# Performance work log

Hardware: AMD Instinct MI355X
Metric: run time of the kernel (lower is better)

The kernel has to match this reference:

```python
import jax, jax.numpy as jnp
import numpy as np

N_A, N_C, N_L = 50000, 10000, 10000
HID = 128


def _gatv2(x_src, x_dst, src, dst, ea, Wl, bl, Wr, br, We, att, bias, H):
    # GATv2Conv (PyG) bipartite, edge_dim=1, concat=False (mean over heads), eval mode (no dropout)
    C = bias.shape[0]
    n_dst = x_dst.shape[0]
    xl = (x_src @ Wl + bl).reshape(-1, H, C)      # [N_src, H, C]
    xr = (x_dst @ Wr + br).reshape(-1, H, C)      # [N_dst, H, C]
    e = jax.nn.leaky_relu(xl[src] + xr[dst] + (ea @ We).reshape(-1, H, C), 0.2)  # [E,H,C]
    logit = jnp.einsum('ehc,hc->eh', e, att)      # [E,H]
    m = jax.ops.segment_max(logit, dst, num_segments=n_dst)
    m = jax.lax.stop_gradient(jnp.where(jnp.isfinite(m), m, 0.0))
    ex = jnp.exp(logit - m[dst])
    denom = jax.ops.segment_sum(ex, dst, num_segments=n_dst)
    alpha = ex / (denom[dst] + 1e-16)             # segment softmax over incoming edges
    out = jax.ops.segment_sum(alpha[:, :, None] * xl[src], dst, num_segments=n_dst)
    return out.mean(axis=1) + bias                # concat=False -> head mean + bias


def setup_inputs() -> dict:
    key = jax.random.key(0)
    ks = iter(jax.random.split(key, 80))
    def rn(shape, s=1.0):
        return jax.random.normal(next(ks), shape, jnp.float32) * s
    inp = {}
    inp['x_asset'] = rn((N_A, 512))
    inp['x_creator'] = rn((N_C, 2))
    inp['x_licensee'] = rn((N_L, 1))
    # edges: (name, E, src_max, dst_max)
    edges = [('cb', 50000, N_A, N_C), ('lt', 100000, N_A, N_L), ('sim', 200000, N_A, N_A),
             ('fw', 100000, N_A, N_A), ('rcb', 50000, N_C, N_A), ('rlt', 100000, N_L, N_A)]
    for name, E, smax, dmax in edges:
        inp[f'{name}_src'] = jax.random.randint(next(ks), (E,), 0, smax, jnp.int32)
        inp[f'{name}_dst'] = jax.random.randint(next(ks), (E,), 0, dmax, jnp.int32)
        inp[f'ea_{name}'] = rn((E, 1))
    w = 0.05  # param scale
    inp['Wp_a'] = rn((512, HID), w); inp['bp_a'] = rn((HID,), w)
    inp['Wp_c'] = rn((2, HID), w);   inp['bp_c'] = rn((HID,), w)
    inp['Wp_l'] = rn((1, HID), w);   inp['bp_l'] = rn((HID,), w)
    # layer 1: heads=2, stacked over the 6 relations
    H1 = 2
    inp['Wl1'] = rn((6, HID, H1 * HID), w); inp['bl1'] = rn((6, H1 * HID), w)
    inp['Wr1'] = rn((6, HID, H1 * HID), w); inp['br1'] = rn((6, H1 * HID), w)
    inp['We1'] = rn((6, 1, H1 * HID), w)
    inp['att1'] = rn((6, H1, HID), w); inp['bias1'] = rn((6, HID), w)
    # layer 2: heads=1
    inp['Wl2'] = rn((6, HID, HID), w); inp['bl2'] = rn((6, HID), w)
    inp['Wr2'] = rn((6, HID, HID), w); inp['br2'] = rn((6, HID), w)
    inp['We2'] = rn((6, 1, HID), w)
    inp['att2'] = rn((6, 1, HID), w); inp['bias2'] = rn((6, HID), w)
    inp['Wc1'] = rn((HID, HID), w); inp['bc1'] = rn((HID,), w)
    inp['Wc2'] = rn((HID, 3), w);   inp['bc2'] = rn((3,), w)
    inp['query_asset_index'] = 123
    return inp


def reference(x_asset, x_creator, x_licensee, Wp_a, bp_a, Wp_c, bp_c, Wp_l, bp_l,
              Wl1, bl1, Wr1, br1, We1, att1, bias1,
              Wl2, bl2, Wr2, br2, We2, att2, bias2,
              Wc1, bc1, Wc2, bc2,
              ea_cb, ea_lt, ea_sim, ea_fw, ea_rcb, ea_rlt,
              cb_src, cb_dst, lt_src, lt_dst, sim_src, sim_dst,
              fw_src, fw_dst, rcb_src, rcb_dst, rlt_src, rlt_dst,
              query_asset_index):
    x = {'Asset': x_asset @ Wp_a + bp_a,
         'Creator': x_creator @ Wp_c + bp_c,
         'Licensee': x_licensee @ Wp_l + bp_l}
    rels = [('Asset', 'Creator', cb_src, cb_dst, ea_cb),
            ('Asset', 'Licensee', lt_src, lt_dst, ea_lt),
            ('Asset', 'Asset', sim_src, sim_dst, ea_sim),
            ('Asset', 'Asset', fw_src, fw_dst, ea_fw),
            ('Creator', 'Asset', rcb_src, rcb_dst, ea_rcb),
            ('Licensee', 'Asset', rlt_src, rlt_dst, ea_rlt)]

    def hetero_layer(x, Wl, bl, Wr, br, We, att, bias, H):
        out = {k: jnp.zeros((v.shape[0], HID), v.dtype) for k, v in x.items()}
        for i, (st, dt, s, d, ea) in enumerate(rels):  # HeteroConv aggr='sum'
            out[dt] = out[dt] + _gatv2(x[st], x[dt], s, d, ea,
                                       Wl[i], bl[i], Wr[i], br[i], We[i], att[i], bias[i], H)
        return out

    x = hetero_layer(x, Wl1, bl1, Wr1, br1, We1, att1, bias1, 2)
    x = {k: jax.nn.relu(v) for k, v in x.items()}  # eval: dropout is identity
    x = hetero_layer(x, Wl2, bl2, Wr2, br2, We2, att2, bias2, 1)
    x = {k: jax.nn.relu(v) for k, v in x.items()}
    a = x['Asset'][query_asset_index]
    return jax.nn.relu(a @ Wc1 + bc1) @ Wc2 + bc2
```

## Files before the change

kernel.cpp:

```cpp
#include <hip/hip_runtime.h>
#include <math.h>

#define FAMAX 64
#define FCMAX 32
#define FLMAX 32
#define N1MAX 512
#define N2MAX 128
#define PROJB 128
#define SCANB 512
#define PFB   96

struct Inputs {
  const float *x_asset, *x_creator, *x_licensee;
  const float *Wp_a,*bp_a,*Wp_c,*bp_c,*Wp_l,*bp_l;
  const float *Wl1,*bl1,*Wr1,*br1,*We1,*att1,*bias1;
  const float *Wl2,*bl2,*Wr2,*br2,*We2,*att2,*bias2;
  const float *Wc1,*bc1,*Wc2,*bc2;
};

struct Edges {
  const int *cb_s,*cb_d;  const float* ea_cb;  int Ecb;
  const int *lt_s,*lt_d;  const float* ea_lt;  int Elt;
  const int *sim_s,*sim_d;const float* ea_sim; int Esim;
  const int *fw_s,*fw_d;  const float* ea_fw;  int Efw;
  const int *rcb_s,*rcb_d;const float* ea_rcb; int Ercb;
  const int *rlt_s,*rlt_d;const float* ea_rlt; int Erlt;
};

struct WSP {
  int* cnt;
  int* nf;
  int* l2rel; int* l2src; float* l2ea; int* l2slot;
  int* l1rel; int* l1src; int* l1dslot; float* l1ea;
  float* xr1a;
  float* xr1c;
  float* xr1l;
  float* xl1e;
  float* logit1;
  float *x1a,*x1c,*x1l;
  float* xl2e;
  float* logit2;
};

__device__ __forceinline__ float leaky(float x){ return x > 0.f ? x : 0.2f*x; }

__device__ __forceinline__ int fsearch(const int* list, int n, int v){
  for (int k=0;k<n;k++) if (list[k]==v) return k;
  return -1;
}

__device__ __forceinline__ float pf4(const float* p, int n, int gt, int gs){
  float s = 0.f;
  const float4* p4 = (const float4*)p;
  int n4 = n >> 2;
  for (int i = gt; i < n4; i += gs){ float4 v = p4[i]; s += v.x+v.y+v.z+v.w; }
  return s;
}

__device__ __forceinline__ void proj256(int type, int node, const Inputs& in,
                                        float* h0, float* xs, float* part){
  int t = threadIdx.x;
  if (type == 0){
    xs[t]       = in.x_asset[(size_t)node*512 + t];
    xs[t + 256] = in.x_asset[(size_t)node*512 + t + 256];
    __syncthreads();
    int j = t & 127, g2 = t >> 7;
    float acc = 0.f;
    const float* W = in.Wp_a + (size_t)g2*256*128 + j;
    const float* xg = xs + g2*256;
    for (int k=0;k<256;k++) acc = fmaf(xg[k], W[(size_t)k*128], acc);
    part[t] = acc;
    __syncthreads();
    if (t < 128) h0[t] = in.bp_a[t] + part[t] + part[128 + t];
  } else if (type == 1){
    if (t < 128)
      h0[t] = in.bp_c[t] + in.x_creator[node*2]*in.Wp_c[t]
            + in.x_creator[node*2+1]*in.Wp_c[128+t];
  } else {
    if (t < 128)
      h0[t] = in.bp_l[t] + in.x_licensee[node]*in.Wp_l[t];
  }
  __syncthreads();
}

__device__ __forceinline__ void l2hit(int rel, int s, float e, WSP& w){
  int k = atomicAdd(&w.cnt[0], 1);
  if (k < N2MAX){ w.l2rel[k]=rel; w.l2src[k]=s; w.l2ea[k]=e; }
}

__device__ __forceinline__ void l2scan_rel(int rel, const int* sp, const int* dp,
                                           const float* ep, int E, int q,
                                           int gt, int gs, WSP& w){
  int nq = E >> 2;
  const int4* d4 = (const int4*)dp;
  for (int i = gt; i < nq; i += gs){
    int4 d = d4[i];
    int j = i << 2;
    if (d.x == q) l2hit(rel, sp[j],   ep[j],   w);
    if (d.y == q) l2hit(rel, sp[j+1], ep[j+1], w);
    if (d.z == q) l2hit(rel, sp[j+2], ep[j+2], w);
    if (d.w == q) l2hit(rel, sp[j+3], ep[j+3], w);
  }
  int base = nq << 2, tail = E - base;
  if (gt < tail){
    int j = base + gt;
    if (dp[j] == q) l2hit(rel, sp[j], ep[j], w);
  }
}

__device__ __forceinline__ void l1hit(int rel, int s, int slot, float e, WSP& w){
  int k = atomicAdd(&w.cnt[4], 1);
  if (k < N1MAX){ w.l1rel[k]=rel; w.l1src[k]=s; w.l1dslot[k]=slot; w.l1ea[k]=e; }
}

__device__ __forceinline__ void l1scan_rel(int rel, const int* sp, const int* dp,
                                           const float* ep, int E,
                                           const int* flist, int fn,
                                           int gt, int gs, WSP& w){
  int nq = E >> 2;
  const int4* d4 = (const int4*)dp;
  for (int i = gt; i < nq; i += gs){
    int4 d = d4[i];
    int j = i << 2;
    int s0 = fsearch(flist, fn, d.x); if (s0>=0) l1hit(rel, sp[j],   s0, ep[j],   w);
    int s1 = fsearch(flist, fn, d.y); if (s1>=0) l1hit(rel, sp[j+1], s1, ep[j+1], w);
    int s2 = fsearch(flist, fn, d.z); if (s2>=0) l1hit(rel, sp[j+2], s2, ep[j+2], w);
    int s3 = fsearch(flist, fn, d.w); if (s3>=0) l1hit(rel, sp[j+3], s3, ep[j+3], w);
  }
  int base = nq << 2, tail = E - base;
  if (gt < tail){
    int j = base + gt;
    int s0 = fsearch(flist, fn, dp[j]);
    if (s0>=0) l1hit(rel, sp[j], s0, ep[j], w);
  }
}

__global__ void __launch_bounds__(256) k1(Edges eg, Inputs in, const int* qptr,
                                          WSP w, int scanB){
  if ((int)blockIdx.x >= scanB){
    int gt = (blockIdx.x - scanB)*256 + threadIdx.x, gs = PFB*256;
    float s = 0.f;
    s += pf4(in.Wp_a, 512*128, gt, gs);
    s += pf4(in.Wr1, 6*128*256, gt, gs);
    s += pf4(in.Wl1, 6*128*256, gt, gs);
    s += pf4(in.Wr2, 6*128*128, gt, gs);
    s += pf4(in.Wl2, 6*128*128, gt, gs);
    s += pf4(in.Wc1, 128*128, gt, gs);
    s += pf4(in.We1, 6*256, gt, gs);
    s += pf4(in.att1, 6*256, gt, gs);
    s += pf4(in.bl1, 6*256, gt, gs);
    s += pf4(in.br1, 6*256, gt, gs);
    s += pf4(in.bias1, 6*128, gt, gs);
    s += pf4(in.We2, 6*128, gt, gs);
    s += pf4(in.att2, 6*128, gt, gs);
    s += pf4(in.bias2, 6*128, gt, gs);
    s += pf4(in.bl2, 6*128, gt, gs);
    s += pf4(in.br2, 6*128, gt, gs);
    s += pf4(in.Wc2, 128*3, gt, gs);
    s += pf4(in.bc1, 128, gt, gs);
    asm volatile("" :: "v"(s));
    return;
  }
  int q = qptr[0];
  int gt = blockIdx.x*256 + threadIdx.x, gs = scanB*256;
  l2scan_rel(2, eg.sim_s, eg.sim_d, eg.ea_sim, eg.Esim, q, gt, gs, w);
  l2scan_rel(3, eg.fw_s,  eg.fw_d,  eg.ea_fw,  eg.Efw,  q, gt, gs, w);
  l2scan_rel(4, eg.rcb_s, eg.rcb_d, eg.ea_rcb, eg.Ercb, q, gt, gs, w);
  l2scan_rel(5, eg.rlt_s, eg.rlt_d, eg.ea_rlt, eg.Erlt, q, gt, gs, w);
}

__global__ void __launch_bounds__(256) k2(Inputs in, Edges eg, WSP w, const int* qptr){
  __shared__ float xs[512], part[256], h0[128];
  __shared__ int s_fa[FAMAX], s_fc[FCMAX], s_fl[FLMAX];
  __shared__ int s_nf[3];
  __shared__ int s_l2rel[N2MAX], s_l2src[N2MAX], s_l2slot[N2MAX];
  int b = blockIdx.x, t = threadIdx.x;
  int q = qptr[0];
  int n2 = min(w.cnt[0], N2MAX);
  for (int i=t; i<n2; i+=256){ s_l2rel[i]=w.l2rel[i]; s_l2src[i]=w.l2src[i]; }
  __syncthreads();
  if (t==0){
    int nfa=0,nfc=0,nfl=0;
    s_fa[nfa++]=q;
    for (int i=0;i<n2;i++){
      int rel=s_l2rel[i], src=s_l2src[i], s=-1;
      if (rel<=3){ s=fsearch(s_fa,nfa,src); if (s<0 && nfa<FAMAX){ s=nfa; s_fa[nfa++]=src; } }
      else if (rel==4){ s=fsearch(s_fc,nfc,src); if (s<0 && nfc<FCMAX){ s=nfc; s_fc[nfc++]=src; } }
      else { s=fsearch(s_fl,nfl,src); if (s<0 && nfl<FLMAX){ s=nfl; s_fl[nfl++]=src; } }
      s_l2slot[i]=s;
    }
    s_nf[0]=nfa; s_nf[1]=nfc; s_nf[2]=nfl;
    if (b==0){
      w.nf[0]=nfa; w.nf[1]=nfc; w.nf[2]=nfl;
      for (int i=0;i<n2;i++) w.l2slot[i]=s_l2slot[i];
    }
  }
  __syncthreads();
  int nfa=s_nf[0], nfc=s_nf[1], nfl=s_nf[2];
  if (b < PROJB){
    int nf = nfa+nfc+nfl;
    if (b < nf){
      int type, slot, node;
      if (b<nfa){ type=0; slot=b; node=s_fa[slot]; }
      else if (b<nfa+nfc){ type=1; slot=b-nfa; node=s_fc[slot]; }
      else { type=2; slot=b-nfa-nfc; node=s_fl[slot]; }
      proj256(type, node, in, h0, xs, part);
      if (type==0){
        for (int rr=0; rr<4; rr++){
          int r = 2+rr;
          float acc = in.br1[r*256+t];
          const float* W = in.Wr1 + (size_t)r*128*256 + t;
          for (int c=0;c<128;c++) acc = fmaf(h0[c], W[(size_t)c*256], acc);
          w.xr1a[((size_t)slot*4+rr)*256 + t] = acc;
        }
      } else if (type==1){
        float acc = in.br1[t];
        const float* W = in.Wr1 + t;
        for (int c=0;c<128;c++) acc = fmaf(h0[c], W[(size_t)c*256], acc);
        w.xr1c[(size_t)slot*256+t] = acc;
      } else {
        float acc = in.br1[256+t];
        const float* W = in.Wr1 + (size_t)128*256 + t;
        for (int c=0;c<128;c++) acc = fmaf(h0[c], W[(size_t)c*256], acc);
        w.xr1l[(size_t)slot*256+t] = acc;
      }
    }
    return;
  }
  int gt = (b-PROJB)*256 + t, gs = SCANB*256;
  l1scan_rel(0, eg.cb_s,  eg.cb_d,  eg.ea_cb,  eg.Ecb,  s_fc, nfc, gt, gs, w);
  l1scan_rel(1, eg.lt_s,  eg.lt_d,  eg.ea_lt,  eg.Elt,  s_fl, nfl, gt, gs, w);
  l1scan_rel(2, eg.sim_s, eg.sim_d, eg.ea_sim, eg.Esim, s_fa, nfa, gt, gs, w);
  l1scan_rel(3, eg.fw_s,  eg.fw_d,  eg.ea_fw,  eg.Efw,  s_fa, nfa, gt, gs, w);
  l1scan_rel(4, eg.rcb_s, eg.rcb_d, eg.ea_rcb, eg.Ercb, s_fa, nfa, gt, gs, w);
  l1scan_rel(5, eg.rlt_s, eg.rlt_d, eg.ea_rlt, eg.Erlt, s_fa, nfa, gt, gs, w);
}

__global__ void __launch_bounds__(256) k3(Inputs in, WSP w){
  __shared__ float xs[512], part[256], h0[128];
  __shared__ float pr[4];
  int t = threadIdx.x;
  int n1 = min(w.cnt[4], N1MAX);
  for (int e = blockIdx.x; e < n1; e += gridDim.x){
    int rel = w.l1rel[e], src = w.l1src[e], dslot = w.l1dslot[e];
    float ea = w.l1ea[e];
    int stype = (rel<=3)?0:(rel==4?1:2);
    proj256(stype, src, in, h0, xs, part);
    float xl1 = in.bl1[rel*256+t];
    {
      const float* W = in.Wl1 + (size_t)rel*128*256 + t;
      for (int c=0;c<128;c++) xl1 = fmaf(h0[c], W[(size_t)c*256], xl1);
    }
    w.xl1e[(size_t)e*256+t] = xl1;
    float xr1 = (rel==0) ? w.xr1c[(size_t)dslot*256+t]
              : (rel==1) ? w.xr1l[(size_t)dslot*256+t]
              : w.xr1a[((size_t)dslot*4 + (rel-2))*256 + t];
    float ev = leaky(xl1 + xr1 + ea*in.We1[rel*256+t]);
    float rd = ev * in.att1[(rel*2 + (t>>7))*128 + (t&127)];
    for (int off=32; off; off>>=1) rd += __shfl_down(rd, off);
    if ((t&63)==0) pr[t>>6] = rd;
    __syncthreads();
    if (t==0){ w.logit1[2*e]=pr[0]+pr[1]; w.logit1[2*e+1]=pr[2]+pr[3]; }
    __syncthreads();
  }
}

__global__ void __launch_bounds__(256) k4a(Inputs in, WSP w){
  __shared__ int   s_key[N1MAX];
  __shared__ float s_lg0[N1MAX], s_lg1[N1MAX];
  __shared__ int   s_list[4][N1MAX];
  __shared__ int   s_c[4];
  __shared__ float sA[256];
  int b = blockIdx.x, t = threadIdx.x;
  int nfa = w.nf[0], nfc = w.nf[1], nfl = w.nf[2];
  int nf = nfa+nfc+nfl;
  if (b >= nf) return;
  int type, slot;
  if (b<nfa){ type=0; slot=b; }
  else if (b<nfa+nfc){ type=1; slot=b-nfa; }
  else { type=2; slot=b-nfa-nfc; }
  int n1 = min(w.cnt[4], N1MAX);
  if (t<4) s_c[t]=0;
  __syncthreads();
  for (int i=t;i<n1;i+=256){
    s_key[i] = (w.l1rel[i]<<6) | w.l1dslot[i];
    float2 L = ((const float2*)w.logit1)[i];
    s_lg0[i] = L.x; s_lg1[i] = L.y;
  }
  __syncthreads();
  int r0,r1;
  if (type==0){ r0=2;r1=5; } else if (type==1){ r0=0;r1=0; } else { r0=1;r1=1; }
  for (int i=t;i<n1;i+=256){
    int key=s_key[i], rel=key>>6, sl=key&63;
    if (sl==slot && rel>=r0 && rel<=r1){
      int li = rel - r0;
      int pos = atomicAdd(&s_c[li],1);
      s_list[li][pos]=i;
    }
  }
  __syncthreads();
  int j = t&127, h = t>>7;
  const float* lg = h ? s_lg1 : s_lg0;
  float out = 0.f;
  for (int r=r0;r<=r1;r++){
    int li = r-r0, c = s_c[li];
    float av = 0.f;
    if (c>0){
      const int* lst = s_list[li];
      float m=-INFINITY;
      for (int o=0;o<c;o++) m = fmaxf(m, lg[lst[o]]);
      float d=0.f, a=0.f;
      for (int o=0;o<c;o++){
        int i = lst[o];
        float e = expf(lg[i]-m);
        d += e;
        a = fmaf(e, w.xl1e[(size_t)i*256 + h*128 + j], a);
      }
      av = a/(d+1e-16f);
    }
    sA[t] = av;
    __syncthreads();
    if (t<128) out += in.bias1[r*128+j] + 0.5f*(sA[j]+sA[j+128]);
    __syncthreads();
  }
  if (t<128){
    float v = fmaxf(out, 0.f);
    if (type==0) w.x1a[(size_t)slot*128+j]=v;
    else if (type==1) w.x1c[(size_t)slot*128+j]=v;
    else w.x1l[(size_t)slot*128+j]=v;
  }
}

__global__ void __launch_bounds__(256) k4b(Inputs in, WSP w){
  __shared__ float xq[128], xsrc[128], px[256], pl[256];
  __shared__ float pr[2];
  int e = blockIdx.x, t = threadIdx.x;
  int n2 = min(w.cnt[0], N2MAX);
  if (e >= n2) return;
  int rel = w.l2rel[e], slot = w.l2slot[e];
  float ea = w.l2ea[e];
  if (slot < 0){
    if (t<128) w.xl2e[(size_t)e*128+t]=0.f;
    if (t==0) w.logit2[e]=-INFINITY;
    return;
  }
  const float* xb = (rel<=3)? w.x1a : (rel==4? w.x1c : w.x1l);
  if (t<128){ xq[t] = w.x1a[t]; xsrc[t] = xb[(size_t)slot*128+t]; }
  __syncthreads();
  int j = t&127, g = t>>7;
  float axr=0.f, axl=0.f;
  {
    const float* Wr = in.Wr2 + (size_t)rel*128*128 + j;
    const float* Wl = in.Wl2 + (size_t)rel*128*128 + j;
    for (int c=g*64; c<g*64+64; c++){
      axr = fmaf(xq[c],   Wr[(size_t)c*128], axr);
      axl = fmaf(xsrc[c], Wl[(size_t)c*128], axl);
    }
  }
  px[t]=axr; pl[t]=axl;
  __syncthreads();
  float rd = 0.f;
  if (t<128){
    float xr2 = in.br2[rel*128+j] + px[j] + px[j+128];
    float xl2 = in.bl2[rel*128+j] + pl[j] + pl[j+128];
    w.xl2e[(size_t)e*128+j] = xl2;
    float ev = leaky(xl2 + xr2 + ea*in.We2[rel*128+j]);
    rd = ev * in.att2[rel*128+j];
  }
  for (int off=32;off;off>>=1) rd += __shfl_down(rd,off);
  if ((t&63)==0 && t<128) pr[t>>6]=rd;
  __syncthreads();
  if (t==0) w.logit2[e] = pr[0]+pr[1];
}

__global__ void __launch_bounds__(256) k4c(Inputs in, WSP w, float* outp){
  __shared__ float x2[128], hid[128], part[256];
  __shared__ int   s_rel[N2MAX];
  __shared__ float s_lg[N2MAX];
  int t = threadIdx.x;
  int n2 = min(w.cnt[0], N2MAX);
  for (int i=t;i<n2;i+=256){ s_rel[i]=w.l2rel[i]; s_lg[i]=w.logit2[i]; }
  __syncthreads();
  if (t<128){
    float o=0.f;
    for (int r=2;r<=5;r++){
      o += in.bias2[r*128+t];
      float m=-INFINITY;
      for (int i=0;i<n2;i++) if (s_rel[i]==r) m=fmaxf(m,s_lg[i]);
      if (m==-INFINITY) continue;
      float d=0.f, acc=0.f;
      for (int i=0;i<n2;i++) if (s_rel[i]==r){
        float e=expf(s_lg[i]-m);
        d+=e;
        acc=fmaf(e, w.xl2e[(size_t)i*128+t], acc);
      }
      o += acc/(d+1e-16f);
    }
    x2[t]=fmaxf(o,0.f);
  }
  __syncthreads();
  int j = t&127, g = t>>7;
  float a=0.f;
  for (int c=g*64;c<g*64+64;c++) a=fmaf(x2[c], in.Wc1[(size_t)c*128+j], a);
  part[t]=a;
  __syncthreads();
  if (t<128) hid[t]=fmaxf(in.bc1[t]+part[t]+part[t+128], 0.f);
  __syncthreads();
  if (t<3){
    float r=in.bc2[t];
    for (int c=0;c<128;c++) r=fmaf(hid[c], in.Wc2[c*3+t], r);
    outp[t]=r;
  }
}

extern "C" void kernel_launch(void* const* d_in, const int* in_sizes, int n_in,
                              void* d_out, int out_size, void* d_ws, size_t ws_size,
                              hipStream_t stream){
  Inputs in;
  in.x_asset   = (const float*)d_in[0];
  in.x_creator = (const float*)d_in[1];
  in.x_licensee= (const float*)d_in[2];
  Edges eg;
  eg.cb_s =(const int*)d_in[3];  eg.cb_d =(const int*)d_in[4];  eg.ea_cb =(const float*)d_in[5];  eg.Ecb = in_sizes[3];
  eg.lt_s =(const int*)d_in[6];  eg.lt_d =(const int*)d_in[7];  eg.ea_lt =(const float*)d_in[8];  eg.Elt = in_sizes[6];
  eg.sim_s=(const int*)d_in[9];  eg.sim_d=(const int*)d_in[10]; eg.ea_sim=(const float*)d_in[11]; eg.Esim= in_sizes[9];
  eg.fw_s =(const int*)d_in[12]; eg.fw_d =(const int*)d_in[13]; eg.ea_fw =(const float*)d_in[14]; eg.Efw = in_sizes[12];
  eg.rcb_s=(const int*)d_in[15]; eg.rcb_d=(const int*)d_in[16]; eg.ea_rcb=(const float*)d_in[17]; eg.Ercb= in_sizes[15];
  eg.rlt_s=(const int*)d_in[18]; eg.rlt_d=(const int*)d_in[19]; eg.ea_rlt=(const float*)d_in[20]; eg.Erlt= in_sizes[18];
  in.Wp_a=(const float*)d_in[21]; in.bp_a=(const float*)d_in[22];
  in.Wp_c=(const float*)d_in[23]; in.bp_c=(const float*)d_in[24];
  in.Wp_l=(const float*)d_in[25]; in.bp_l=(const float*)d_in[26];
  in.Wl1=(const float*)d_in[27]; in.bl1=(const float*)d_in[28];
  in.Wr1=(const float*)d_in[29]; in.br1=(const float*)d_in[30];
  in.We1=(const float*)d_in[31]; in.att1=(const float*)d_in[32]; in.bias1=(const float*)d_in[33];
  in.Wl2=(const float*)d_in[34]; in.bl2=(const float*)d_in[35];
  in.Wr2=(const float*)d_in[36]; in.br2=(const float*)d_in[37];
  in.We2=(const float*)d_in[38]; in.att2=(const float*)d_in[39]; in.bias2=(const float*)d_in[40];
  in.Wc1=(const float*)d_in[41]; in.bc1=(const float*)d_in[42];
  in.Wc2=(const float*)d_in[43]; in.bc2=(const float*)d_in[44];
  const int* qptr = (const int*)d_in[45];
  float* outp = (float*)d_out;

  char* p = (char*)d_ws;
  auto carve = [&](size_t n)->char*{ char* r = p; p += ((n + 255) & ~(size_t)255); return r; };
  WSP w;
  w.cnt  = (int*)carve(16*4);
  w.nf   = (int*)carve(3*4);
  w.l2rel=(int*)carve(N2MAX*4); w.l2src=(int*)carve(N2MAX*4);
  w.l2ea=(float*)carve(N2MAX*4); w.l2slot=(int*)carve(N2MAX*4);
  w.l1rel=(int*)carve(N1MAX*4); w.l1src=(int*)carve(N1MAX*4);
  w.l1dslot=(int*)carve(N1MAX*4); w.l1ea=(float*)carve(N1MAX*4);
  w.xr1a=(float*)carve((size_t)FAMAX*4*256*4);
  w.xr1c=(float*)carve((size_t)FCMAX*256*4);
  w.xr1l=(float*)carve((size_t)FLMAX*256*4);
  w.xl1e=(float*)carve((size_t)N1MAX*256*4);
  w.logit1=(float*)carve((size_t)N1MAX*2*4);
  w.x1a=(float*)carve((size_t)FAMAX*128*4);
  w.x1c=(float*)carve((size_t)FCMAX*128*4);
  w.x1l=(float*)carve((size_t)FLMAX*128*4);
  w.xl2e=(float*)carve((size_t)N2MAX*128*4);
  w.logit2=(float*)carve(N2MAX*4);

  hipMemsetAsync(w.cnt, 0, 64, stream);

  int quad2 = (eg.Esim + eg.Efw + eg.Ercb + eg.Erlt)/4 + 1;
  int b1 = (quad2 + 255)/256; if (b1 > 1024) b1 = 1024;
  k1<<<b1 + PFB, 256, 0, stream>>>(eg, in, qptr, w, b1);
  k2<<<PROJB + SCANB, 256, 0, stream>>>(in, eg, w, qptr);
  k3<<<256, 256, 0, stream>>>(in, w);
  k4a<<<FAMAX + FCMAX + FLMAX, 256, 0, stream>>>(in, w);
  k4b<<<N2MAX, 256, 0, stream>>>(in, w);
  k4c<<<1, 256, 0, stream>>>(in, w, outp);
}
```

Before: 288.1 us.

## Fuse layer-1 aggregation, layer-2 edge compute and classifier into one kernel

The three tail kernels k4a, k4b and k4c become a single kernel, k45. Each layer-2 edge block now recomputes the layer-1 aggregated features it needs, for the query asset and its own source node, instead of reading them from a separate pass. The final softmax and classifier run in whichever block finishes last, detected with an atomic counter and threadfence. This removes two kernel launches and their gaps, at the cost of redundant per-block recomputation of the query node's aggregation and a counter in cnt[12] that relies on the memset being reset each call.

```diff
diff --git a/kernel.cpp b/kernel.cpp
--- a/kernel.cpp
+++ b/kernel.cpp
@@ -37,7 +37,6 @@
   float* xr1l;
   float* xl1e;
   float* logit1;
-  float *x1a,*x1c,*x1l;
   float* xl2e;
   float* logit2;
 };
@@ -265,150 +264,165 @@
   }
 }
 
-__global__ void __launch_bounds__(256) k4a(Inputs in, WSP w){
+__global__ void __launch_bounds__(256) k45(Inputs in, WSP w, float* outp){
   __shared__ int   s_key[N1MAX];
   __shared__ float s_lg0[N1MAX], s_lg1[N1MAX];
-  __shared__ int   s_list[4][N1MAX];
-  __shared__ int   s_c[4];
+  __shared__ int   s_lq[4][N1MAX], s_ls[4][N1MAX];
+  __shared__ int   s_c[8];
   __shared__ float sA[256];
-  int b = blockIdx.x, t = threadIdx.x;
-  int nfa = w.nf[0], nfc = w.nf[1], nfl = w.nf[2];
-  int nf = nfa+nfc+nfl;
-  if (b >= nf) return;
-  int type, slot;
-  if (b<nfa){ type=0; slot=b; }
-  else if (b<nfa+nfc){ type=1; slot=b-nfa; }
-  else { type=2; slot=b-nfa-nfc; }
-  int n1 = min(w.cnt[4], N1MAX);
-  if (t<4) s_c[t]=0;
-  __syncthreads();
-  for (int i=t;i<n1;i+=256){
-    s_key[i] = (w.l1rel[i]<<6) | w.l1dslot[i];
-    float2 L = ((const float2*)w.logit1)[i];
-    s_lg0[i] = L.x; s_lg1[i] = L.y;
-  }
-  __syncthreads();
-  int r0,r1;
-  if (type==0){ r0=2;r1=5; } else if (type==1){ r0=0;r1=0; } else { r0=1;r1=1; }
-  for (int i=t;i<n1;i+=256){
-    int key=s_key[i], rel=key>>6, sl=key&63;
-    if (sl==slot && rel>=r0 && rel<=r1){
-      int li = rel - r0;
-      int pos = atomicAdd(&s_c[li],1);
-      s_list[li][pos]=i;
-    }
-  }
-  __syncthreads();
-  int j = t&127, h = t>>7;
-  const float* lg = h ? s_lg1 : s_lg0;
-  float out = 0.f;
-  for (int r=r0;r<=r1;r++){
-    int li = r-r0, c = s_c[li];
-    float av = 0.f;
-    if (c>0){
-      const int* lst = s_list[li];
-      float m=-INFINITY;
-      for (int o=0;o<c;o++) m = fmaxf(m, lg[lst[o]]);
-      float d=0.f, a=0.f;
-      for (int o=0;o<c;o++){
-        int i = lst[o];
-        float e = expf(lg[i]-m);
-        d += e;
-        a = fmaf(e, w.xl1e[(size_t)i*256 + h*128 + j], a);
-      }
-      av = a/(d+1e-16f);
-    }
-    sA[t] = av;
-    __syncthreads();
-    if (t<128) out += in.bias1[r*128+j] + 0.5f*(sA[j]+sA[j+128]);
-    __syncthreads();
-  }
-  if (t<128){
-    float v = fmaxf(out, 0.f);
-    if (type==0) w.x1a[(size_t)slot*128+j]=v;
-    else if (type==1) w.x1c[(size_t)slot*128+j]=v;
-    else w.x1l[(size_t)slot*128+j]=v;
-  }
-}
-
-__global__ void __launch_bounds__(256) k4b(Inputs in, WSP w){
-  __shared__ float xq[128], xsrc[128], px[256], pl[256];
+  __shared__ float xq[128], xsrc[128];
+  __shared__ float px[256], pl[256];
   __shared__ float pr[2];
+  __shared__ int   s_last;
   int e = blockIdx.x, t = threadIdx.x;
   int n2 = min(w.cnt[0], N2MAX);
-  if (e >= n2) return;
-  int rel = w.l2rel[e], slot = w.l2slot[e];
-  float ea = w.l2ea[e];
-  if (slot < 0){
+  bool active = (e < n2);
+  int rel = 2, slot = -1; float ea = 0.f;
+  if (active){ rel = w.l2rel[e]; slot = w.l2slot[e]; ea = w.l2ea[e]; }
+  if (active && slot >= 0){
+    int n1 = min(w.cnt[4], N1MAX);
+    if (t<8) s_c[t]=0;
+    __syncthreads();
+    for (int i=t;i<n1;i+=256){
+      s_key[i] = (w.l1rel[i]<<6) | w.l1dslot[i];
+      float2 L = ((const float2*)w.logit1)[i];
+      s_lg0[i]=L.x; s_lg1[i]=L.y;
+    }
+    __syncthreads();
+    int sr0 = (rel<=3)?2:(rel==4?0:1);
+    int snr = (rel<=3)?4:1;
+    bool srcq = (rel<=3 && slot==0);
+    for (int i=t;i<n1;i+=256){
+      int key=s_key[i], r=key>>6, sl=key&63;
+      if (sl==0 && r>=2){ int p=atomicAdd(&s_c[r-2],1); s_lq[r-2][p]=i; }
+      if (!srcq && sl==slot && r>=sr0 && r<sr0+snr){
+        int p=atomicAdd(&s_c[4+r-sr0],1); s_ls[r-sr0][p]=i;
+      }
+    }
+    __syncthreads();
+    int j=t&127, h=t>>7;
+    const float* lg = h ? s_lg1 : s_lg0;
+    {
+      float out=0.f;
+      for (int ri=0;ri<4;ri++){
+        int r=2+ri, c=s_c[ri];
+        float av=0.f;
+        if (c>0){
+          const int* lst=s_lq[ri];
+          float m=-INFINITY;
+          for (int o=0;o<c;o++) m=fmaxf(m, lg[lst[o]]);
+          float d=0.f,a=0.f;
+          for (int o=0;o<c;o++){
+            int i=lst[o];
+            float ex=expf(lg[i]-m);
+            d+=ex;
+            a=fmaf(ex, w.xl1e[(size_t)i*256 + h*128 + j], a);
+          }
+          av=a/(d+1e-16f);
+        }
+        sA[t]=av; __syncthreads();
+        if (t<128) out += in.bias1[r*128+j] + 0.5f*(sA[j]+sA[j+128]);
+        __syncthreads();
+      }
+      if (t<128) xq[j]=fmaxf(out,0.f);
+      __syncthreads();
+    }
+    if (srcq){
+      if (t<128) xsrc[t]=xq[t];
+      __syncthreads();
+    } else {
+      float out=0.f;
+      for (int ri=0;ri<snr;ri++){
+        int r=sr0+ri, c=s_c[4+ri];
+        float av=0.f;
+        if (c>0){
+          const int* lst=s_ls[ri];
+          float m=-INFINITY;
+          for (int o=0;o<c;o++) m=fmaxf(m, lg[lst[o]]);
+          float d=0.f,a=0.f;
+          for (int o=0;o<c;o++){
+            int i=lst[o];
+            float ex=expf(lg[i]-m);
+            d+=ex;
+            a=fmaf(ex, w.xl1e[(size_t)i*256 + h*128 + j], a);
+          }
+          av=a/(d+1e-16f);
+        }
+        sA[t]=av; __syncthreads();
+        if (t<128) out += in.bias1[r*128+j] + 0.5f*(sA[j]+sA[j+128]);
+        __syncthreads();
+      }
+      if (t<128) xsrc[j]=fmaxf(out,0.f);
+      __syncthreads();
+    }
+    int g=t>>7;
+    float axr=0.f, axl=0.f;
+    {
+      const float* Wr = in.Wr2 + (size_t)rel*128*128 + j;
+      const float* Wl = in.Wl2 + (size_t)rel*128*128 + j;
+      for (int c=g*64;c<g*64+64;c++){
+        axr=fmaf(xq[c],   Wr[(size_t)c*128], axr);
+        axl=fmaf(xsrc[c], Wl[(size_t)c*128], axl);
+      }
+    }
+    px[t]=axr; pl[t]=axl;
+    __syncthreads();
+    float rd=0.f;
+    if (t<128){
+      float xr2 = in.br2[rel*128+j] + px[j] + px[j+128];
+      float xl2 = in.bl2[rel*128+j] + pl[j] + pl[j+128];
+      w.xl2e[(size_t)e*128+j]=xl2;
+      float ev = leaky(xl2 + xr2 + ea*in.We2[rel*128+j]);
+      rd = ev * in.att2[rel*128+j];
+    }
+    for (int off=32;off;off>>=1) rd += __shfl_down(rd,off);
+    if ((t&63)==0 && t<128) pr[t>>6]=rd;
+    __syncthreads();
+    if (t==0) w.logit2[e]=pr[0]+pr[1];
+  } else if (active){
     if (t<128) w.xl2e[(size_t)e*128+t]=0.f;
     if (t==0) w.logit2[e]=-INFINITY;
-    return;
-  }
-  const float* xb = (rel<=3)? w.x1a : (rel==4? w.x1c : w.x1l);
-  if (t<128){ xq[t] = w.x1a[t]; xsrc[t] = xb[(size_t)slot*128+t]; }
-  __syncthreads();
-  int j = t&127, g = t>>7;
-  float axr=0.f, axl=0.f;
-  {
-    const float* Wr = in.Wr2 + (size_t)rel*128*128 + j;
-    const float* Wl = in.Wl2 + (size_t)rel*128*128 + j;
-    for (int c=g*64; c<g*64+64; c++){
-      axr = fmaf(xq[c],   Wr[(size_t)c*128], axr);
-      axl = fmaf(xsrc[c], Wl[(size_t)c*128], axl);
-    }
-  }
-  px[t]=axr; pl[t]=axl;
-  __syncthreads();
-  float rd = 0.f;
-  if (t<128){
-    float xr2 = in.br2[rel*128+j] + px[j] + px[j+128];
-    float xl2 = in.bl2[rel*128+j] + pl[j] + pl[j+128];
-    w.xl2e[(size_t)e*128+j] = xl2;
-    float ev = leaky(xl2 + xr2 + ea*in.We2[rel*128+j]);
-    rd = ev * in.att2[rel*128+j];
-  }
-  for (int off=32;off;off>>=1) rd += __shfl_down(rd,off);
-  if ((t&63)==0 && t<128) pr[t>>6]=rd;
-  __syncthreads();
-  if (t==0) w.logit2[e] = pr[0]+pr[1];
-}
-
-__global__ void __launch_bounds__(256) k4c(Inputs in, WSP w, float* outp){
-  __shared__ float x2[128], hid[128], part[256];
-  __shared__ int   s_rel[N2MAX];
-  __shared__ float s_lg[N2MAX];
-  int t = threadIdx.x;
-  int n2 = min(w.cnt[0], N2MAX);
-  for (int i=t;i<n2;i+=256){ s_rel[i]=w.l2rel[i]; s_lg[i]=w.logit2[i]; }
+  }
+  __syncthreads();
+  if (t==0){
+    __threadfence();
+    int v = atomicAdd(&w.cnt[12], 1);
+    s_last = (v == (int)gridDim.x - 1) ? 1 : 0;
+  }
+  __syncthreads();
+  if (!s_last) return;
+  if (t==0) __threadfence();
+  __syncthreads();
+  for (int i=t;i<n2;i+=256){ s_key[i]=w.l2rel[i]; s_lg0[i]=w.logit2[i]; }
   __syncthreads();
   if (t<128){
     float o=0.f;
     for (int r=2;r<=5;r++){
       o += in.bias2[r*128+t];
       float m=-INFINITY;
-      for (int i=0;i<n2;i++) if (s_rel[i]==r) m=fmaxf(m,s_lg[i]);
+      for (int i=0;i<n2;i++) if (s_key[i]==r) m=fmaxf(m,s_lg0[i]);
       if (m==-INFINITY) continue;
       float d=0.f, acc=0.f;
-      for (int i=0;i<n2;i++) if (s_rel[i]==r){
-        float e=expf(s_lg[i]-m);
-        d+=e;
-        acc=fmaf(e, w.xl2e[(size_t)i*128+t], acc);
+      for (int i=0;i<n2;i++) if (s_key[i]==r){
+        float ex=expf(s_lg0[i]-m);
+        d+=ex;
+        acc=fmaf(ex, w.xl2e[(size_t)i*128+t], acc);
       }
       o += acc/(d+1e-16f);
     }
-    x2[t]=fmaxf(o,0.f);
-  }
-  __syncthreads();
-  int j = t&127, g = t>>7;
+    xq[t]=fmaxf(o,0.f);
+  }
+  __syncthreads();
+  int j=t&127, g=t>>7;
   float a=0.f;
-  for (int c=g*64;c<g*64+64;c++) a=fmaf(x2[c], in.Wc1[(size_t)c*128+j], a);
-  part[t]=a;
-  __syncthreads();
-  if (t<128) hid[t]=fmaxf(in.bc1[t]+part[t]+part[t+128], 0.f);
+  for (int c=g*64;c<g*64+64;c++) a=fmaf(xq[c], in.Wc1[(size_t)c*128+j], a);
+  px[t]=a;
+  __syncthreads();
+  if (t<128) xsrc[t]=fmaxf(in.bc1[t]+px[t]+px[t+128], 0.f);
   __syncthreads();
   if (t<3){
     float r=in.bc2[t];
-    for (int c=0;c<128;c++) r=fmaf(hid[c], in.Wc2[c*3+t], r);
+    for (int c=0;c<128;c++) r=fmaf(xsrc[c], in.Wc2[c*3+t], r);
     outp[t]=r;
   }
 }
@@ -455,9 +469,6 @@
   w.xr1l=(float*)carve((size_t)FLMAX*256*4);
   w.xl1e=(float*)carve((size_t)N1MAX*256*4);
   w.logit1=(float*)carve((size_t)N1MAX*2*4);
-  w.x1a=(float*)carve((size_t)FAMAX*128*4);
-  w.x1c=(float*)carve((size_t)FCMAX*128*4);
-  w.x1l=(float*)carve((size_t)FLMAX*128*4);
   w.xl2e=(float*)carve((size_t)N2MAX*128*4);
   w.logit2=(float*)carve(N2MAX*4);
 
@@ -468,7 +479,5 @@
   k1<<<b1 + PFB, 256, 0, stream>>>(eg, in, qptr, w, b1);
   k2<<<PROJB + SCANB, 256, 0, stream>>>(in, eg, w, qptr);
   k3<<<256, 256, 0, stream>>>(in, w);
-  k4a<<<FAMAX + FCMAX + FLMAX, 256, 0, stream>>>(in, w);
-  k4b<<<N2MAX, 256, 0, stream>>>(in, w);
-  k4c<<<1, 256, 0, stream>>>(in, w, outp);
-}
+  k45<<<N2MAX, 256, 0, stream>>>(in, w, outp);
+}
```

New measurement: 286.7 us. About the same (-0.5%).
